# Kernel optimization log

Hardware: AMD Instinct MI355X
Metric: run time of the kernel (lower is better)

Reference implementation:

```python
import jax, jax.numpy as jnp
import numpy as np

H = 2048
V = 32000
N = 2048  # batch*seq tokens
IGNORE_INDEX = -100
TEMPERATURE = 1.0
W_HARD = 0.5
W_SOFT = 0.5


def setup_inputs() -> dict:
    key = jax.random.key(0)
    k1, k2, k3, k4, k5 = jax.random.split(key, 5)
    student_input = jax.random.normal(k1, (N, H // 2), dtype=jnp.float32)
    teacher_input = jax.random.normal(k2, (N, H), dtype=jnp.float32)
    target = jax.random.randint(k3, (N,), 0, V, dtype=jnp.int64)
    # learned params: Linear(in, out=V, bias=False) -> weight shape (V, in)
    student_weight = jax.random.normal(k4, (V, H // 2), dtype=jnp.float32) * 0.02
    teacher_weight = jax.random.normal(k5, (V, H), dtype=jnp.float32) * 0.02
    return {
        "student_input": student_input,
        "teacher_input": teacher_input,
        "student_weight": student_weight,
        "teacher_weight": teacher_weight,
        "target": target,
    }


def reference(student_input, teacher_input, student_weight, teacher_weight, target):
    # Linear projections to vocab (teacher under no_grad in torch)
    student_logits = (student_input @ student_weight.T).astype(jnp.float32)  # (N, V)
    teacher_logits = jax.lax.stop_gradient(
        (teacher_input @ teacher_weight.T).astype(jnp.float32)
    )  # (N, V)

    # Hard loss: cross-entropy with ignore_index, mean over valid tokens
    log_probs = jax.nn.log_softmax(student_logits, axis=-1)
    valid = target != IGNORE_INDEX
    safe_tgt = jnp.where(valid, target, 0)
    nll = -jnp.take_along_axis(log_probs, safe_tgt[:, None], axis=-1)[:, 0]
    n_valid = jnp.maximum(valid.sum(), 1)
    hard_loss = jnp.sum(jnp.where(valid, nll, 0.0)) / n_valid

    # Soft loss: Jensen-Shannon divergence with batchmean reduction
    sl = student_logits / TEMPERATURE
    tl = teacher_logits / TEMPERATURE
    student_probs = jax.nn.softmax(sl, axis=-1)
    teacher_probs = jax.nn.softmax(tl, axis=-1)
    log_mean = jnp.log((student_probs + teacher_probs) * 0.5)
    log_sp = jnp.log(student_probs)
    log_tp = jnp.log(teacher_probs)
    n = sl.shape[0]
    # kl_div(log_mean, log_p, log_target=True, batchmean) = sum(p*(log_p - log_mean))/n
    student_kl = jnp.sum(student_probs * (log_sp - log_mean)) / n
    teacher_kl = jnp.sum(teacher_probs * (log_tp - log_mean)) / n
    jsd_loss = (student_kl + teacher_kl) * 0.5

    return W_HARD * hard_loss + W_SOFT * jsd_loss
```

## Files before the change

### kernel.cpp

```cpp
#include <hip/hip_runtime.h>

#define VOCAB 32000
#define NTOK 2048
#define IGNORE_INDEX (-100)

typedef unsigned short u16;
typedef unsigned int u32;
typedef __bf16 bf16x8 __attribute__((ext_vector_type(8)));
typedef float floatx4 __attribute__((ext_vector_type(4)));

__device__ __forceinline__ u16 f2bf(float f) {
    u32 u = __float_as_uint(f);
    u32 r = u + 0x7fffu + ((u >> 16) & 1u);
    return (u16)(r >> 16);
}
__device__ __forceinline__ float bf2f(u32 lo16) {
    return __uint_as_float(lo16 << 16);
}

__global__ __launch_bounds__(256) void cvt_kernel(const float* __restrict__ in,
                                                  u16* __restrict__ out, int n4) {
    int i = blockIdx.x * 256 + threadIdx.x;
    if (i >= n4) return;
    float4 v = ((const float4*)in)[i];
    ushort4 o;
    o.x = f2bf(v.x); o.y = f2bf(v.y); o.z = f2bf(v.z); o.w = f2bf(v.w);
    ((ushort4*)out)[i] = o;
}

__global__ __launch_bounds__(256) void zero_kernel(float* __restrict__ p, int n) {
    int i = blockIdx.x * 256 + threadIdx.x;
    if (i < n) p[i] = 0.f;
}

__global__ __launch_bounds__(256) void gemm_bt_kernel(
    const u16* __restrict__ A, const u16* __restrict__ B, u16* __restrict__ C,
    float* __restrict__ rowsum, int M, int N, int K)
{
    __shared__ u16 lds[2 * 128 * 64];
    u16* lds_a = lds;
    u16* lds_b = lds + 128 * 64;

    const int tid  = threadIdx.x;
    const int lane = tid & 63;
    const int wave = tid >> 6;
    const int bm = blockIdx.x * 128;
    const int bn = blockIdx.y * 128;
    const int wm = (wave >> 1) * 64;
    const int wn = (wave & 1) * 64;

    floatx4 acc[4][4] = {};

    const int l8 = lane >> 3;
    const int c8 = lane & 7;
    const int srow = wave * 8 + l8;
    const int scol = ((c8 ^ l8) << 3);
    const u16* ap0 = A + (size_t)(bm + srow) * K + scol;
    const u16* ap1 = ap0 + (size_t)32 * K;
    const u16* ap2 = ap0 + (size_t)64 * K;
    const u16* ap3 = ap0 + (size_t)96 * K;
    const u16* bp0 = B + (size_t)(bn + srow) * K + scol;
    const u16* bp1 = bp0 + (size_t)32 * K;
    const u16* bp2 = bp0 + (size_t)64 * K;
    const u16* bp3 = bp0 + (size_t)96 * K;

    for (int k0 = 0; k0 < K; k0 += 64) {
        __builtin_amdgcn_global_load_lds((const __attribute__((address_space(1))) u32*)ap0,
            (__attribute__((address_space(3))) u32*)(lds_a + wave * 512 + 0 * 2048), 16, 0, 0);
        __builtin_amdgcn_global_load_lds((const __attribute__((address_space(1))) u32*)ap1,
            (__attribute__((address_space(3))) u32*)(lds_a + wave * 512 + 1 * 2048), 16, 0, 0);
        __builtin_amdgcn_global_load_lds((const __attribute__((address_space(1))) u32*)ap2,
            (__attribute__((address_space(3))) u32*)(lds_a + wave * 512 + 2 * 2048), 16, 0, 0);
        __builtin_amdgcn_global_load_lds((const __attribute__((address_space(1))) u32*)ap3,
            (__attribute__((address_space(3))) u32*)(lds_a + wave * 512 + 3 * 2048), 16, 0, 0);
        __builtin_amdgcn_global_load_lds((const __attribute__((address_space(1))) u32*)bp0,
            (__attribute__((address_space(3))) u32*)(lds_b + wave * 512 + 0 * 2048), 16, 0, 0);
        __builtin_amdgcn_global_load_lds((const __attribute__((address_space(1))) u32*)bp1,
            (__attribute__((address_space(3))) u32*)(lds_b + wave * 512 + 1 * 2048), 16, 0, 0);
        __builtin_amdgcn_global_load_lds((const __attribute__((address_space(1))) u32*)bp2,
            (__attribute__((address_space(3))) u32*)(lds_b + wave * 512 + 2 * 2048), 16, 0, 0);
        __builtin_amdgcn_global_load_lds((const __attribute__((address_space(1))) u32*)bp3,
            (__attribute__((address_space(3))) u32*)(lds_b + wave * 512 + 3 * 2048), 16, 0, 0);
        ap0 += 64; ap1 += 64; ap2 += 64; ap3 += 64;
        bp0 += 64; bp1 += 64; bp2 += 64; bp3 += 64;
        __syncthreads();
#pragma unroll
        for (int s = 0; s < 2; ++s) {
            const int swz = (((s * 4) + (lane >> 4)) ^ (lane & 7)) << 3;
            bf16x8 af[4], bq[4];
#pragma unroll
            for (int i = 0; i < 4; ++i)
                af[i] = *(const bf16x8*)(lds_a + (wm + i * 16 + (lane & 15)) * 64 + swz);
#pragma unroll
            for (int j = 0; j < 4; ++j)
                bq[j] = *(const bf16x8*)(lds_b + (wn + j * 16 + (lane & 15)) * 64 + swz);
#pragma unroll
            for (int i = 0; i < 4; ++i)
#pragma unroll
                for (int j = 0; j < 4; ++j)
                    acc[i][j] = __builtin_amdgcn_mfma_f32_16x16x32_bf16(af[i], bq[j], acc[i][j], 0, 0, 0);
        }
        __syncthreads();
    }

    const int q = lane >> 4;
    const int cl = lane & 15;
#pragma unroll
    for (int i = 0; i < 4; ++i) {
#pragma unroll
        for (int j = 0; j < 4; ++j) {
            const int col = wn + j * 16 + cl;
#pragma unroll
            for (int r = 0; r < 4; ++r) {
                const int row = wm + i * 16 + q * 4 + r;
                lds[row * 128 + ((((col >> 3) ^ (row & 15)) << 3) | (col & 7))] =
                    f2bf(acc[i][j][r]);
            }
        }
    }
    __syncthreads();

#pragma unroll
    for (int p = 0; p < 8; ++p) {
        const int idx = p * 256 + tid;
        const int row = idx >> 4;
        const int ch  = idx & 15;
        uint4 v = *(const uint4*)(lds + row * 128 + ((ch ^ (row & 15)) << 3));
        *(uint4*)(C + (size_t)(bm + row) * N + bn + ch * 8) = v;
        float se = __expf(bf2f(v.x & 0xffffu)) + __expf(bf2f(v.x >> 16))
                 + __expf(bf2f(v.y & 0xffffu)) + __expf(bf2f(v.y >> 16))
                 + __expf(bf2f(v.z & 0xffffu)) + __expf(bf2f(v.z >> 16))
                 + __expf(bf2f(v.w & 0xffffu)) + __expf(bf2f(v.w >> 16));
        se += __shfl_xor(se, 1);
        se += __shfl_xor(se, 2);
        se += __shfl_xor(se, 4);
        se += __shfl_xor(se, 8);
        if ((tid & 15) == 0) atomicAdd(rowsum + bm + row, se);
    }
}

__global__ __launch_bounds__(256) void rowstats_kernel(
    const u16* __restrict__ Ls, const u16* __restrict__ Lt,
    const float* __restrict__ rowsum, const int* __restrict__ tgt,
    float* __restrict__ rows)
{
    const int n    = blockIdx.x;
    const int tid  = threadIdx.x;
    const int lane = tid & 63;
    const int wave = tid >> 6;

    const u16* lsrow = Ls + (size_t)n * VOCAB;
    const u16* ltrow = Lt + (size_t)n * VOCAB;
    const uint4* ls4 = (const uint4*)lsrow;
    const uint4* lt4 = (const uint4*)ltrow;
    const int V8 = VOCAB / 8;

    const float lse_s = __logf(rowsum[n]);
    const float lse_t = __logf(rowsum[NTOK + n]);

    float jacc = 0.f;
    for (int v = tid; v < V8; v += 256) {
        uint4 a = ls4[v], b = lt4[v];
        u32 pa[4] = {a.x, a.y, a.z, a.w};
        u32 pb[4] = {b.x, b.y, b.z, b.w};
#pragma unroll
        for (int qq = 0; qq < 4; ++qq) {
            float lsp0 = bf2f(pa[qq] & 0xffffu) - lse_s, lsp1 = bf2f(pa[qq] >> 16) - lse_s;
            float ltp0 = bf2f(pb[qq] & 0xffffu) - lse_t, ltp1 = bf2f(pb[qq] >> 16) - lse_t;
            float sp0 = __expf(lsp0), sp1 = __expf(lsp1);
            float tp0 = __expf(ltp0), tp1 = __expf(ltp1);
            float lm0 = __logf(0.5f * (sp0 + tp0));
            float lm1 = __logf(0.5f * (sp1 + tp1));
            jacc += sp0 * (lsp0 - lm0) + tp0 * (ltp0 - lm0);
            jacc += sp1 * (lsp1 - lm1) + tp1 * (ltp1 - lm1);
        }
    }
#pragma unroll
    for (int off = 32; off > 0; off >>= 1) jacc += __shfl_down(jacc, off);
    __shared__ float jsh[4];
    if (lane == 0) jsh[wave] = jacc;
    __syncthreads();
    if (tid == 0) {
        float j = jsh[0] + jsh[1] + jsh[2] + jsh[3];
        int t = tgt[n];
        bool valid = (t != IGNORE_INDEX);
        float nll = 0.f;
        if (valid) nll = lse_s - bf2f((u32)lsrow[t]);
        rows[n * 3 + 0] = nll;
        rows[n * 3 + 1] = valid ? 1.f : 0.f;
        rows[n * 3 + 2] = j;
    }
}

__global__ __launch_bounds__(256) void final_kernel(const float* __restrict__ rows,
                                                    float* __restrict__ out) {
    const int tid = threadIdx.x;
    float a = 0.f, b = 0.f, c = 0.f;
    for (int i = tid; i < NTOK; i += 256) {
        a += rows[i * 3]; b += rows[i * 3 + 1]; c += rows[i * 3 + 2];
    }
#pragma unroll
    for (int off = 32; off > 0; off >>= 1) {
        a += __shfl_down(a, off);
        b += __shfl_down(b, off);
        c += __shfl_down(c, off);
    }
    __shared__ float sh[4][3];
    const int lane = tid & 63, wave = tid >> 6;
    if (lane == 0) { sh[wave][0] = a; sh[wave][1] = b; sh[wave][2] = c; }
    __syncthreads();
    if (tid == 0) {
        a = sh[0][0] + sh[1][0] + sh[2][0] + sh[3][0];
        b = sh[0][1] + sh[1][1] + sh[2][1] + sh[3][1];
        c = sh[0][2] + sh[1][2] + sh[2][2] + sh[3][2];
        float nv = fmaxf(b, 1.f);
        out[0] = 0.5f * (a / nv) + 0.25f * (c / (float)NTOK);
    }
}

extern "C" void kernel_launch(void* const* d_in, const int* in_sizes, int n_in,
                              void* d_out, int out_size, void* d_ws, size_t ws_size,
                              hipStream_t stream)
{
    const float* s_in = (const float*)d_in[0];
    const float* t_in = (const float*)d_in[1];
    const float* s_w  = (const float*)d_in[2];
    const float* t_w  = (const float*)d_in[3];
    const int*   tgt  = (const int*)d_in[4];

    u16* sA = (u16*)d_ws;
    u16* tA = sA + (size_t)NTOK * 1024;
    u16* sW = tA + (size_t)NTOK * 2048;
    u16* tW = sW + (size_t)VOCAB * 1024;
    u16* Ls = tW + (size_t)VOCAB * 2048;
    u16* Lt = Ls + (size_t)NTOK * VOCAB;
    float* rows   = (float*)(Lt + (size_t)NTOK * VOCAB);
    float* rowsum = rows + NTOK * 3;

    int n4;
    n4 = NTOK * 1024 / 4;  cvt_kernel<<<(n4 + 255) / 256, 256, 0, stream>>>(s_in, sA, n4);
    n4 = NTOK * 2048 / 4;  cvt_kernel<<<(n4 + 255) / 256, 256, 0, stream>>>(t_in, tA, n4);
    n4 = VOCAB * 1024 / 4; cvt_kernel<<<(n4 + 255) / 256, 256, 0, stream>>>(s_w, sW, n4);
    n4 = VOCAB * 2048 / 4; cvt_kernel<<<(n4 + 255) / 256, 256, 0, stream>>>(t_w, tW, n4);
    zero_kernel<<<(2 * NTOK + 255) / 256, 256, 0, stream>>>(rowsum, 2 * NTOK);

    dim3 g(NTOK / 128, VOCAB / 128);
    gemm_bt_kernel<<<g, 256, 0, stream>>>(sA, sW, Ls, rowsum,        NTOK, VOCAB, 1024);
    gemm_bt_kernel<<<g, 256, 0, stream>>>(tA, tW, Lt, rowsum + NTOK, NTOK, VOCAB, 2048);

    rowstats_kernel<<<NTOK, 256, 0, stream>>>(Ls, Lt, rowsum, tgt, rows);
    final_kernel<<<1, 256, 0, stream>>>(rows, (float*)d_out);
}
```

Baseline: 1.043 ms.

## Rewrite GEMM as 256x256 tiles with double-buffered LDS and interleaved prefetch

The logits GEMM moves from 128x128 tiles with 4 waves and a single LDS buffer to 256x256 tiles with 8 waves, a double-buffered 128KB LDS, and a 1D grid remapped so eight consecutive blocks share a column of weight tiles. Global-to-LDS loads for the next k-step are issued between MFMA phases, with explicit barriers, waitcnts and s_setprio raising priority around the MFMA phases. This targets load latency and global traffic per FLOP. The cost is higher register and LDS pressure, which limits occupancy, and a 1000-block grid, which may leave some CUs with uneven work.

After: 961.3 us. 1.08x faster.

```diff
diff --git a/kernel.cpp b/kernel.cpp
--- a/kernel.cpp
+++ b/kernel.cpp
@@ -33,99 +33,169 @@
     if (i < n) p[i] = 0.f;
 }
 
-__global__ __launch_bounds__(256) void gemm_bt_kernel(
+__global__ __launch_bounds__(512, 2) void gemm_bt_kernel(
     const u16* __restrict__ A, const u16* __restrict__ B, u16* __restrict__ C,
     float* __restrict__ rowsum, int M, int N, int K)
 {
-    __shared__ u16 lds[2 * 128 * 64];
-    u16* lds_a = lds;
-    u16* lds_b = lds + 128 * 64;
+    __shared__ u16 lds[65536];
 
     const int tid  = threadIdx.x;
     const int lane = tid & 63;
     const int wave = tid >> 6;
-    const int bm = blockIdx.x * 128;
-    const int bn = blockIdx.y * 128;
-    const int wm = (wave >> 1) * 64;
-    const int wn = (wave & 1) * 64;
-
-    floatx4 acc[4][4] = {};
-
-    const int l8 = lane >> 3;
-    const int c8 = lane & 7;
-    const int srow = wave * 8 + l8;
-    const int scol = ((c8 ^ l8) << 3);
-    const u16* ap0 = A + (size_t)(bm + srow) * K + scol;
-    const u16* ap1 = ap0 + (size_t)32 * K;
-    const u16* ap2 = ap0 + (size_t)64 * K;
-    const u16* ap3 = ap0 + (size_t)96 * K;
-    const u16* bp0 = B + (size_t)(bn + srow) * K + scol;
-    const u16* bp1 = bp0 + (size_t)32 * K;
-    const u16* bp2 = bp0 + (size_t)64 * K;
-    const u16* bp3 = bp0 + (size_t)96 * K;
-
-    for (int k0 = 0; k0 < K; k0 += 64) {
-        __builtin_amdgcn_global_load_lds((const __attribute__((address_space(1))) u32*)ap0,
-            (__attribute__((address_space(3))) u32*)(lds_a + wave * 512 + 0 * 2048), 16, 0, 0);
-        __builtin_amdgcn_global_load_lds((const __attribute__((address_space(1))) u32*)ap1,
-            (__attribute__((address_space(3))) u32*)(lds_a + wave * 512 + 1 * 2048), 16, 0, 0);
-        __builtin_amdgcn_global_load_lds((const __attribute__((address_space(1))) u32*)ap2,
-            (__attribute__((address_space(3))) u32*)(lds_a + wave * 512 + 2 * 2048), 16, 0, 0);
-        __builtin_amdgcn_global_load_lds((const __attribute__((address_space(1))) u32*)ap3,
-            (__attribute__((address_space(3))) u32*)(lds_a + wave * 512 + 3 * 2048), 16, 0, 0);
-        __builtin_amdgcn_global_load_lds((const __attribute__((address_space(1))) u32*)bp0,
-            (__attribute__((address_space(3))) u32*)(lds_b + wave * 512 + 0 * 2048), 16, 0, 0);
-        __builtin_amdgcn_global_load_lds((const __attribute__((address_space(1))) u32*)bp1,
-            (__attribute__((address_space(3))) u32*)(lds_b + wave * 512 + 1 * 2048), 16, 0, 0);
-        __builtin_amdgcn_global_load_lds((const __attribute__((address_space(1))) u32*)bp2,
-            (__attribute__((address_space(3))) u32*)(lds_b + wave * 512 + 2 * 2048), 16, 0, 0);
-        __builtin_amdgcn_global_load_lds((const __attribute__((address_space(1))) u32*)bp3,
-            (__attribute__((address_space(3))) u32*)(lds_b + wave * 512 + 3 * 2048), 16, 0, 0);
-        ap0 += 64; ap1 += 64; ap2 += 64; ap3 += 64;
-        bp0 += 64; bp1 += 64; bp2 += 64; bp3 += 64;
-        __syncthreads();
-#pragma unroll
-        for (int s = 0; s < 2; ++s) {
-            const int swz = (((s * 4) + (lane >> 4)) ^ (lane & 7)) << 3;
-            bf16x8 af[4], bq[4];
-#pragma unroll
-            for (int i = 0; i < 4; ++i)
-                af[i] = *(const bf16x8*)(lds_a + (wm + i * 16 + (lane & 15)) * 64 + swz);
-#pragma unroll
-            for (int j = 0; j < 4; ++j)
-                bq[j] = *(const bf16x8*)(lds_b + (wn + j * 16 + (lane & 15)) * 64 + swz);
-#pragma unroll
-            for (int i = 0; i < 4; ++i)
-#pragma unroll
-                for (int j = 0; j < 4; ++j)
-                    acc[i][j] = __builtin_amdgcn_mfma_f32_16x16x32_bf16(af[i], bq[j], acc[i][j], 0, 0, 0);
-        }
-        __syncthreads();
-    }
-
-    const int q = lane >> 4;
+    const int wr = wave >> 2;
+    const int wc = wave & 3;
+
+    const int nx = gridDim.x >> 3;
+    const int wg = (blockIdx.x & 7) * nx + (blockIdx.x >> 3);
+    const int bm = (wg & 7) * 256;
+    const int bn = (wg >> 3) * 256;
+
+    const int nk = K >> 6;
+
+    const int l8 = lane >> 3, c8 = lane & 7;
+    const u16* ap[4]; const u16* bp[4];
+#pragma unroll
+    for (int h = 0; h < 2; ++h)
+#pragma unroll
+        for (int qq = 0; qq < 2; ++qq) {
+            const int r = h * 128 + qq * 64 + wave * 8 + l8;
+            ap[h * 2 + qq] = A + (size_t)(bm + r) * K + ((c8 ^ l8) << 3);
+            bp[h * 2 + qq] = B + (size_t)(bn + r) * K + ((c8 ^ l8) << 3);
+        }
+    const int du = wave * 512;
+
+#define GLDS(gp, off) __builtin_amdgcn_global_load_lds( \
+        (const __attribute__((address_space(1))) u32*)(gp), \
+        (__attribute__((address_space(3))) u32*)(lds + (off)), 16, 0, 0)
+#define STAGE_A(b) do { \
+        GLDS(ap[0], (b) * 16384 + du);          GLDS(ap[1], (b) * 16384 + 4096 + du); \
+        GLDS(ap[2], (b) * 16384 + 8192 + du);   GLDS(ap[3], (b) * 16384 + 12288 + du); \
+        ap[0] += 64; ap[1] += 64; ap[2] += 64; ap[3] += 64; } while (0)
+#define STAGE_B(b) do { \
+        GLDS(bp[0], 32768 + (b) * 16384 + du);        GLDS(bp[1], 32768 + (b) * 16384 + 4096 + du); \
+        GLDS(bp[2], 32768 + (b) * 16384 + 8192 + du); GLDS(bp[3], 32768 + (b) * 16384 + 12288 + du); \
+        bp[0] += 64; bp[1] += 64; bp[2] += 64; bp[3] += 64; } while (0)
+
+#define BAR()        __builtin_amdgcn_s_barrier()
+#define WAIT_LGKM0() asm volatile("s_waitcnt lgkmcnt(0)" ::: "memory")
+#define WAIT_VM0()   asm volatile("s_waitcnt vmcnt(0)" ::: "memory")
+#define PIN()        __builtin_amdgcn_sched_barrier(0)
+
+    floatx4 acc[8][4] = {};
+    bf16x8 af[4][2], bqA[2][2], bqB[2][2];
+
+    const int rA  = wr * 128 + (lane & 15);
+    const int rB  = wc * 64 + (lane & 15);
+    const int sw0 = (((lane >> 4) + 0) ^ (lane & 7)) << 3;
+    const int sw1 = (((lane >> 4) + 4) ^ (lane & 7)) << 3;
+
+    STAGE_A(0); STAGE_B(0);
+    WAIT_VM0(); BAR();
+
+    for (int ks = 0; ks < nk; ++ks) {
+        const int cb = ks & 1;
+        const u16* As = lds + cb * 16384;
+        const u16* Bs = lds + 32768 + cb * 16384;
+        const bool pf = (ks + 1) < nk;
+
+#pragma unroll
+        for (int m = 0; m < 4; ++m) {
+            af[m][0] = *(const bf16x8*)(As + (rA + m * 16) * 64 + sw0);
+            af[m][1] = *(const bf16x8*)(As + (rA + m * 16) * 64 + sw1);
+        }
+#pragma unroll
+        for (int n = 0; n < 2; ++n) {
+            bqA[n][0] = *(const bf16x8*)(Bs + (rB + n * 16) * 64 + sw0);
+            bqA[n][1] = *(const bf16x8*)(Bs + (rB + n * 16) * 64 + sw1);
+        }
+        if (pf) STAGE_A(cb ^ 1);
+        BAR();
+        WAIT_LGKM0(); PIN();
+        __builtin_amdgcn_s_setprio(1);
+#pragma unroll
+        for (int m = 0; m < 4; ++m)
+#pragma unroll
+            for (int n = 0; n < 2; ++n) {
+                acc[m][n] = __builtin_amdgcn_mfma_f32_16x16x32_bf16(af[m][0], bqA[n][0], acc[m][n], 0, 0, 0);
+                acc[m][n] = __builtin_amdgcn_mfma_f32_16x16x32_bf16(af[m][1], bqA[n][1], acc[m][n], 0, 0, 0);
+            }
+        __builtin_amdgcn_s_setprio(0);
+        BAR();
+
+#pragma unroll
+        for (int n = 0; n < 2; ++n) {
+            bqB[n][0] = *(const bf16x8*)(Bs + (rB + 32 + n * 16) * 64 + sw0);
+            bqB[n][1] = *(const bf16x8*)(Bs + (rB + 32 + n * 16) * 64 + sw1);
+        }
+        if (pf) STAGE_B(cb ^ 1);
+        BAR();
+        WAIT_LGKM0(); PIN();
+        __builtin_amdgcn_s_setprio(1);
+#pragma unroll
+        for (int m = 0; m < 4; ++m)
+#pragma unroll
+            for (int n = 0; n < 2; ++n) {
+                acc[m][n + 2] = __builtin_amdgcn_mfma_f32_16x16x32_bf16(af[m][0], bqB[n][0], acc[m][n + 2], 0, 0, 0);
+                acc[m][n + 2] = __builtin_amdgcn_mfma_f32_16x16x32_bf16(af[m][1], bqB[n][1], acc[m][n + 2], 0, 0, 0);
+            }
+        __builtin_amdgcn_s_setprio(0);
+        BAR();
+
+#pragma unroll
+        for (int m = 0; m < 4; ++m) {
+            af[m][0] = *(const bf16x8*)(As + (rA + 64 + m * 16) * 64 + sw0);
+            af[m][1] = *(const bf16x8*)(As + (rA + 64 + m * 16) * 64 + sw1);
+        }
+        BAR();
+        WAIT_LGKM0(); PIN();
+        __builtin_amdgcn_s_setprio(1);
+#pragma unroll
+        for (int m = 0; m < 4; ++m)
+#pragma unroll
+            for (int n = 0; n < 2; ++n) {
+                acc[m + 4][n] = __builtin_amdgcn_mfma_f32_16x16x32_bf16(af[m][0], bqA[n][0], acc[m + 4][n], 0, 0, 0);
+                acc[m + 4][n] = __builtin_amdgcn_mfma_f32_16x16x32_bf16(af[m][1], bqA[n][1], acc[m + 4][n], 0, 0, 0);
+            }
+        __builtin_amdgcn_s_setprio(0);
+        BAR();
+
+        WAIT_VM0();
+        BAR();
+        __builtin_amdgcn_s_setprio(1);
+#pragma unroll
+        for (int m = 0; m < 4; ++m)
+#pragma unroll
+            for (int n = 0; n < 2; ++n) {
+                acc[m + 4][n + 2] = __builtin_amdgcn_mfma_f32_16x16x32_bf16(af[m][0], bqB[n][0], acc[m + 4][n + 2], 0, 0, 0);
+                acc[m + 4][n + 2] = __builtin_amdgcn_mfma_f32_16x16x32_bf16(af[m][1], bqB[n][1], acc[m + 4][n + 2], 0, 0, 0);
+            }
+        __builtin_amdgcn_s_setprio(0);
+        BAR();
+    }
+
+    __syncthreads();
+    const int q4 = lane >> 4;
     const int cl = lane & 15;
 #pragma unroll
-    for (int i = 0; i < 4; ++i) {
-#pragma unroll
-        for (int j = 0; j < 4; ++j) {
-            const int col = wn + j * 16 + cl;
-#pragma unroll
-            for (int r = 0; r < 4; ++r) {
-                const int row = wm + i * 16 + q * 4 + r;
-                lds[row * 128 + ((((col >> 3) ^ (row & 15)) << 3) | (col & 7))] =
-                    f2bf(acc[i][j][r]);
-            }
-        }
-    }
+    for (int m = 0; m < 8; ++m)
+#pragma unroll
+        for (int n = 0; n < 4; ++n) {
+            const int col = wc * 64 + n * 16 + cl;
+#pragma unroll
+            for (int rr = 0; rr < 4; ++rr) {
+                const int row = wr * 128 + m * 16 + q4 * 4 + rr;
+                lds[row * 256 + ((((col >> 3) ^ (row & 31)) << 3) | (col & 7))] =
+                    f2bf(acc[m][n][rr]);
+            }
+        }
     __syncthreads();
 
 #pragma unroll
-    for (int p = 0; p < 8; ++p) {
-        const int idx = p * 256 + tid;
-        const int row = idx >> 4;
-        const int ch  = idx & 15;
-        uint4 v = *(const uint4*)(lds + row * 128 + ((ch ^ (row & 15)) << 3));
+    for (int p = 0; p < 16; ++p) {
+        const int idx = p * 512 + tid;
+        const int row = idx >> 5;
+        const int ch  = idx & 31;
+        uint4 v = *(const uint4*)(lds + row * 256 + ((ch ^ (row & 31)) << 3));
         *(uint4*)(C + (size_t)(bm + row) * N + bn + ch * 8) = v;
         float se = __expf(bf2f(v.x & 0xffffu)) + __expf(bf2f(v.x >> 16))
                  + __expf(bf2f(v.y & 0xffffu)) + __expf(bf2f(v.y >> 16))
@@ -135,7 +205,8 @@
         se += __shfl_xor(se, 2);
         se += __shfl_xor(se, 4);
         se += __shfl_xor(se, 8);
-        if ((tid & 15) == 0) atomicAdd(rowsum + bm + row, se);
+        se += __shfl_xor(se, 16);
+        if ((tid & 31) == 0) atomicAdd(rowsum + bm + row, se);
     }
 }
 
@@ -244,9 +315,8 @@
     n4 = VOCAB * 2048 / 4; cvt_kernel<<<(n4 + 255) / 256, 256, 0, stream>>>(t_w, tW, n4);
     zero_kernel<<<(2 * NTOK + 255) / 256, 256, 0, stream>>>(rowsum, 2 * NTOK);
 
-    dim3 g(NTOK / 128, VOCAB / 128);
-    gemm_bt_kernel<<<g, 256, 0, stream>>>(sA, sW, Ls, rowsum,        NTOK, VOCAB, 1024);
-    gemm_bt_kernel<<<g, 256, 0, stream>>>(tA, tW, Lt, rowsum + NTOK, NTOK, VOCAB, 2048);
+    gemm_bt_kernel<<<dim3(1000), 512, 0, stream>>>(sA, sW, Ls, rowsum,        NTOK, VOCAB, 1024);
+    gemm_bt_kernel<<<dim3(1000), 512, 0, stream>>>(tA, tW, Lt, rowsum + NTOK, NTOK, VOCAB, 2048);
 
     rowstats_kernel<<<NTOK, 256, 0, stream>>>(Ls, Lt, rowsum, tgt, rows);
     final_kernel<<<1, 256, 0, stream>>>(rows, (float*)d_out);
```

## Use 256x256 GEMM tiles with double-buffered LDS prefetch and grouped block order

Applied to the files above, without the earlier changes.

Rewrites the bf16 GEMM to compute 256x256 output tiles per block (8x8 MFMA accumulators per wave) instead of 128x128. LDS staging is double-buffered so the next K-slice loads and fragment prefetch overlap with MFMA work. A 1D grid is remapped so that groups of 8 row tiles share column tiles, which is meant to improve L2 reuse of the weights. The costs are much higher register pressure (launch_bounds 256,1), one block per CU, and the full 128KB LDS.

After: 1.247 ms. 19.6% more time.

```diff
diff --git a/kernel.cpp b/kernel.cpp
--- a/kernel.cpp
+++ b/kernel.cpp
@@ -33,99 +33,116 @@
     if (i < n) p[i] = 0.f;
 }
 
-__global__ __launch_bounds__(256) void gemm_bt_kernel(
+__global__ __launch_bounds__(256, 1) void gemm_bt_kernel(
     const u16* __restrict__ A, const u16* __restrict__ B, u16* __restrict__ C,
     float* __restrict__ rowsum, int M, int N, int K)
 {
-    __shared__ u16 lds[2 * 128 * 64];
-    u16* lds_a = lds;
-    u16* lds_b = lds + 128 * 64;
+    __shared__ u16 lds[65536];
 
     const int tid  = threadIdx.x;
     const int lane = tid & 63;
     const int wave = tid >> 6;
-    const int bm = blockIdx.x * 128;
-    const int bn = blockIdx.y * 128;
-    const int wm = (wave >> 1) * 64;
-    const int wn = (wave & 1) * 64;
-
-    floatx4 acc[4][4] = {};
-
-    const int l8 = lane >> 3;
-    const int c8 = lane & 7;
-    const int srow = wave * 8 + l8;
-    const int scol = ((c8 ^ l8) << 3);
-    const u16* ap0 = A + (size_t)(bm + srow) * K + scol;
-    const u16* ap1 = ap0 + (size_t)32 * K;
-    const u16* ap2 = ap0 + (size_t)64 * K;
-    const u16* ap3 = ap0 + (size_t)96 * K;
-    const u16* bp0 = B + (size_t)(bn + srow) * K + scol;
-    const u16* bp1 = bp0 + (size_t)32 * K;
-    const u16* bp2 = bp0 + (size_t)64 * K;
-    const u16* bp3 = bp0 + (size_t)96 * K;
-
-    for (int k0 = 0; k0 < K; k0 += 64) {
-        __builtin_amdgcn_global_load_lds((const __attribute__((address_space(1))) u32*)ap0,
-            (__attribute__((address_space(3))) u32*)(lds_a + wave * 512 + 0 * 2048), 16, 0, 0);
-        __builtin_amdgcn_global_load_lds((const __attribute__((address_space(1))) u32*)ap1,
-            (__attribute__((address_space(3))) u32*)(lds_a + wave * 512 + 1 * 2048), 16, 0, 0);
-        __builtin_amdgcn_global_load_lds((const __attribute__((address_space(1))) u32*)ap2,
-            (__attribute__((address_space(3))) u32*)(lds_a + wave * 512 + 2 * 2048), 16, 0, 0);
-        __builtin_amdgcn_global_load_lds((const __attribute__((address_space(1))) u32*)ap3,
-            (__attribute__((address_space(3))) u32*)(lds_a + wave * 512 + 3 * 2048), 16, 0, 0);
-        __builtin_amdgcn_global_load_lds((const __attribute__((address_space(1))) u32*)bp0,
-            (__attribute__((address_space(3))) u32*)(lds_b + wave * 512 + 0 * 2048), 16, 0, 0);
-        __builtin_amdgcn_global_load_lds((const __attribute__((address_space(1))) u32*)bp1,
-            (__attribute__((address_space(3))) u32*)(lds_b + wave * 512 + 1 * 2048), 16, 0, 0);
-        __builtin_amdgcn_global_load_lds((const __attribute__((address_space(1))) u32*)bp2,
-            (__attribute__((address_space(3))) u32*)(lds_b + wave * 512 + 2 * 2048), 16, 0, 0);
-        __builtin_amdgcn_global_load_lds((const __attribute__((address_space(1))) u32*)bp3,
-            (__attribute__((address_space(3))) u32*)(lds_b + wave * 512 + 3 * 2048), 16, 0, 0);
-        ap0 += 64; ap1 += 64; ap2 += 64; ap3 += 64;
-        bp0 += 64; bp1 += 64; bp2 += 64; bp3 += 64;
-        __syncthreads();
-#pragma unroll
-        for (int s = 0; s < 2; ++s) {
-            const int swz = (((s * 4) + (lane >> 4)) ^ (lane & 7)) << 3;
-            bf16x8 af[4], bq[4];
-#pragma unroll
-            for (int i = 0; i < 4; ++i)
-                af[i] = *(const bf16x8*)(lds_a + (wm + i * 16 + (lane & 15)) * 64 + swz);
-#pragma unroll
-            for (int j = 0; j < 4; ++j)
-                bq[j] = *(const bf16x8*)(lds_b + (wn + j * 16 + (lane & 15)) * 64 + swz);
-#pragma unroll
-            for (int i = 0; i < 4; ++i)
-#pragma unroll
-                for (int j = 0; j < 4; ++j)
-                    acc[i][j] = __builtin_amdgcn_mfma_f32_16x16x32_bf16(af[i], bq[j], acc[i][j], 0, 0, 0);
-        }
-        __syncthreads();
-    }
-
-    const int q = lane >> 4;
+    const int wr = wave >> 1;
+    const int wc = wave & 1;
+
+    const int nx = gridDim.x >> 3;
+    const int wg = (blockIdx.x & 7) * nx + (blockIdx.x >> 3);
+    const int bm = (wg & 7) * 256;
+    const int bn = (wg >> 3) * 256;
+
+    const int nk = K >> 6;
+
+    const int l8 = lane >> 3, c8 = lane & 7;
+    const u16* apb = A + (size_t)(bm + wave * 64 + l8) * K + ((c8 ^ l8) << 3);
+    const u16* bpb = B + (size_t)(bn + wave * 64 + l8) * K + ((c8 ^ l8) << 3);
+
+#define GLDS(gp, off) __builtin_amdgcn_global_load_lds( \
+        (const __attribute__((address_space(1))) u32*)(gp), \
+        (__attribute__((address_space(3))) u32*)(lds + (off)), 16, 0, 0)
+#define STAGE(b) do { \
+        _Pragma("unroll") for (int g_ = 0; g_ < 8; ++g_) \
+            GLDS(apb + (size_t)(g_ * 8) * K, (b) * 16384 + wave * 4096 + g_ * 512); \
+        _Pragma("unroll") for (int g_ = 0; g_ < 8; ++g_) \
+            GLDS(bpb + (size_t)(g_ * 8) * K, 32768 + (b) * 16384 + wave * 4096 + g_ * 512); \
+        apb += 64; bpb += 64; } while (0)
+
+#define BAR()      __builtin_amdgcn_s_barrier()
+#define WAIT_VM0() asm volatile("s_waitcnt vmcnt(0)" ::: "memory")
+#define SCHED0()   __builtin_amdgcn_sched_barrier(0)
+
+    floatx4 acc[8][8] = {};
+    bf16x8 afL[4][2], afH[4][2], bqL[4][2], bqH[4][2], afLn[4][2], bqLn[4][2];
+
+    const int rAl = wr * 128 + (lane & 15);
+    const int rBl = wc * 128 + (lane & 15);
+    const int sw0 = (((lane >> 4) + 0) ^ (lane & 7)) << 3;
+    const int sw1 = (((lane >> 4) + 4) ^ (lane & 7)) << 3;
+
+#define LOADF(DST, BUFB, RBASE) do { \
+        _Pragma("unroll") for (int i_ = 0; i_ < 4; ++i_) { \
+            DST[i_][0] = *(const bf16x8*)((BUFB) + ((RBASE) + i_ * 16) * 64 + sw0); \
+            DST[i_][1] = *(const bf16x8*)((BUFB) + ((RBASE) + i_ * 16) * 64 + sw1); \
+        } } while (0)
+
+#define QUAD(MO, NO, AF, BQ) do { \
+        _Pragma("unroll") for (int m_ = 0; m_ < 4; ++m_) \
+        _Pragma("unroll") for (int n_ = 0; n_ < 4; ++n_) { \
+            acc[(MO) + m_][(NO) + n_] = __builtin_amdgcn_mfma_f32_16x16x32_bf16( \
+                AF[m_][0], BQ[n_][0], acc[(MO) + m_][(NO) + n_], 0, 0, 0); \
+            acc[(MO) + m_][(NO) + n_] = __builtin_amdgcn_mfma_f32_16x16x32_bf16( \
+                AF[m_][1], BQ[n_][1], acc[(MO) + m_][(NO) + n_], 0, 0, 0); \
+        } } while (0)
+
+#define BODY(CB, CA, CQ, NA, NQ, PFS, PFR) do { \
+        const u16* As_  = lds + (CB) * 16384; \
+        const u16* Bs_  = lds + 32768 + (CB) * 16384; \
+        const u16* As2_ = lds + ((CB) ^ 1) * 16384; \
+        const u16* Bs2_ = lds + 32768 + ((CB) ^ 1) * 16384; \
+        LOADF(afH, As_, rAl + 64); \
+        LOADF(bqH, Bs_, rBl + 64); \
+        QUAD(0, 0, CA, CQ); \
+        QUAD(0, 4, CA, bqH); \
+        QUAD(4, 0, afH, CQ); \
+        WAIT_VM0(); BAR(); SCHED0(); \
+        if (PFS) STAGE(CB); \
+        if (PFR) { LOADF(NA, As2_, rAl); LOADF(NQ, Bs2_, rBl); } \
+        QUAD(4, 4, afH, bqH); \
+    } while (0)
+
+    STAGE(0);
+    WAIT_VM0(); BAR(); SCHED0();
+    LOADF(afL, lds, rAl);
+    LOADF(bqL, (lds + 32768), rBl);
+    STAGE(1);
+
+    for (int ks = 0; ks < nk; ks += 2) {
+        BODY(0, afL, bqL, afLn, bqLn, (ks + 2) < nk, (ks + 1) < nk);
+        BODY(1, afLn, bqLn, afL, bqL, (ks + 3) < nk, (ks + 2) < nk);
+    }
+
+    __syncthreads();
+    const int q4 = lane >> 4;
     const int cl = lane & 15;
 #pragma unroll
-    for (int i = 0; i < 4; ++i) {
-#pragma unroll
-        for (int j = 0; j < 4; ++j) {
-            const int col = wn + j * 16 + cl;
-#pragma unroll
-            for (int r = 0; r < 4; ++r) {
-                const int row = wm + i * 16 + q * 4 + r;
-                lds[row * 128 + ((((col >> 3) ^ (row & 15)) << 3) | (col & 7))] =
-                    f2bf(acc[i][j][r]);
+    for (int m = 0; m < 8; ++m)
+#pragma unroll
+        for (int n = 0; n < 8; ++n) {
+            const int col = wc * 128 + n * 16 + cl;
+#pragma unroll
+            for (int rr = 0; rr < 4; ++rr) {
+                const int row = wr * 128 + m * 16 + q4 * 4 + rr;
+                lds[row * 256 + ((((col >> 3) ^ (row & 31)) << 3) | (col & 7))] =
+                    f2bf(acc[m][n][rr]);
             }
         }
-    }
-    __syncthreads();
-
-#pragma unroll
-    for (int p = 0; p < 8; ++p) {
+    __syncthreads();
+
+#pragma unroll
+    for (int p = 0; p < 32; ++p) {
         const int idx = p * 256 + tid;
-        const int row = idx >> 4;
-        const int ch  = idx & 15;
-        uint4 v = *(const uint4*)(lds + row * 128 + ((ch ^ (row & 15)) << 3));
+        const int row = idx >> 5;
+        const int ch  = idx & 31;
+        uint4 v = *(const uint4*)(lds + row * 256 + ((ch ^ (row & 31)) << 3));
         *(uint4*)(C + (size_t)(bm + row) * N + bn + ch * 8) = v;
         float se = __expf(bf2f(v.x & 0xffffu)) + __expf(bf2f(v.x >> 16))
                  + __expf(bf2f(v.y & 0xffffu)) + __expf(bf2f(v.y >> 16))
@@ -135,7 +152,8 @@
         se += __shfl_xor(se, 2);
         se += __shfl_xor(se, 4);
         se += __shfl_xor(se, 8);
-        if ((tid & 15) == 0) atomicAdd(rowsum + bm + row, se);
+        se += __shfl_xor(se, 16);
+        if ((tid & 31) == 0) atomicAdd(rowsum + bm + row, se);
     }
 }
 
@@ -244,9 +262,8 @@
     n4 = VOCAB * 2048 / 4; cvt_kernel<<<(n4 + 255) / 256, 256, 0, stream>>>(t_w, tW, n4);
     zero_kernel<<<(2 * NTOK + 255) / 256, 256, 0, stream>>>(rowsum, 2 * NTOK);
 
-    dim3 g(NTOK / 128, VOCAB / 128);
-    gemm_bt_kernel<<<g, 256, 0, stream>>>(sA, sW, Ls, rowsum,        NTOK, VOCAB, 1024);
-    gemm_bt_kernel<<<g, 256, 0, stream>>>(tA, tW, Lt, rowsum + NTOK, NTOK, VOCAB, 2048);
+    gemm_bt_kernel<<<dim3(1000), 256, 0, stream>>>(sA, sW, Ls, rowsum,        NTOK, VOCAB, 1024);
+    gemm_bt_kernel<<<dim3(1000), 256, 0, stream>>>(tA, tW, Lt, rowsum + NTOK, NTOK, VOCAB, 2048);
 
     rowstats_kernel<<<NTOK, 256, 0, stream>>>(Ls, Lt, rowsum, tgt, rows);
     final_kernel<<<1, 256, 0, stream>>>(rows, (float*)d_out);
```
